# Kernel tuning notes

Hardware: AMD Instinct MI355X
Metric: run time of the kernel (lower is better)

The kernel has to match this reference:

```python
import jax, jax.numpy as jnp
import numpy as np

N = 100000

def _gcn_conv(x, W, b, row, col, norm, n_nodes):
    # x: [N, Fin], W: [Fin, Fout]; message = norm * (x W)[row], aggregated at col
    h = x @ W                                  # small GEMM
    msg = h[row] * norm[:, None]               # [E+N, Fout] gather (memory bound)
    out = jax.ops.segment_sum(msg, col, num_segments=n_nodes)
    return out + b

def _norm_coeffs(edge_index, n_nodes):
    # add self-loops, compute symmetric normalization deg^-1/2[row]*deg^-1/2[col]
    loops = jnp.arange(n_nodes, dtype=edge_index.dtype)
    row = jnp.concatenate([edge_index[0], loops])
    col = jnp.concatenate([edge_index[1], loops])
    deg = jax.ops.segment_sum(jnp.ones_like(col, dtype=jnp.float32), col,
                              num_segments=n_nodes)
    dinv = jnp.where(deg > 0, jax.lax.rsqrt(deg), 0.0)
    norm = dinv[row] * dinv[col]
    return row, col, norm

def setup_inputs() -> dict:
    key = jax.random.key(0)
    ks = jax.random.split(key, 4)
    x = jax.random.normal(ks[0], (N, 64), dtype=jnp.float32)
    edge_index = jax.random.randint(ks[1], (2, 1600000), 0, N, dtype=jnp.int64)
    W1 = jax.random.normal(ks[2], (64, 64), dtype=jnp.float32) / np.sqrt(64)
    b1 = jnp.zeros((64,), dtype=jnp.float32)
    W2 = jax.random.normal(ks[3], (64, 64), dtype=jnp.float32) / np.sqrt(64)
    b2 = jnp.zeros((64,), dtype=jnp.float32)
    return {"x": x, "edge_index": edge_index, "W1": W1, "b1": b1, "W2": W2, "b2": b2}

def reference(x, edge_index, W1, b1, W2, b2):
    row, col, norm = _norm_coeffs(edge_index, N)
    h = jax.nn.relu(_gcn_conv(x, W1, b1, row, col, norm, N))
    return _gcn_conv(h, W2, b2, row, col, norm, N)
```

## Files before the change

### kernel.cpp

```cpp
#include <hip/hip_runtime.h>


#define NPB 32
#define BSH 8
#define BSZ 256
#define PTILE 2048
#define CAP 6144
#define PADALLOW 3856
#define CROW (CAP + PADALLOW)

typedef __attribute__((ext_vector_type(8))) short bf16x8;
typedef __attribute__((ext_vector_type(4))) float f32x4;

__device__ __forceinline__ unsigned bf16_rne(float f) {
    unsigned b = __float_as_uint(f);
    return (b + 0x7fffu + ((b >> 16) & 1u)) >> 16;
}
__device__ __forceinline__ float bf16_lo(unsigned u) { return __uint_as_float(u << 16); }
__device__ __forceinline__ float bf16_hi(unsigned u) { return __uint_as_float(u & 0xffff0000u); }

__global__ void k_binit(int* __restrict__ bcur, int NB) {
    int b = blockIdx.x * blockDim.x + threadIdx.x;
    if (b < NB) bcur[b] = b * CAP;
}

__global__ __launch_bounds__(256) void k_part(const int* __restrict__ rowi,
                                              const int* __restrict__ coli,
                                              int E, int N, int NB, int numTiles,
                                              int* __restrict__ bcur,
                                              unsigned* __restrict__ pairs) {
    __shared__ int hist[512];
    __shared__ int base[512];
    int t = threadIdx.x;
    int T = E + N;
    for (int tile = blockIdx.x; tile < numTiles; tile += gridDim.x) {
        int tstart = tile * PTILE;
        int m = min(PTILE, T - tstart);
        for (int b = t; b < NB; b += 256) hist[b] = 0;
        __syncthreads();
        for (int i = t; i < m; i += 256) {
            int g = tstart + i;
            int c = (g < E) ? coli[g] : (g - E);
            atomicAdd(&hist[c >> BSH], 1);
        }
        __syncthreads();
        for (int b = t; b < NB; b += 256) {
            int h = hist[b];
            base[b] = h ? atomicAdd(&bcur[b], h) : 0;
            hist[b] = 0;
        }
        __syncthreads();
        for (int i = t; i < m; i += 256) {
            int g = tstart + i;
            int r, c;
            if (g < E) { r = rowi[g]; c = coli[g]; }
            else       { r = g - E; c = r; }
            int b = c >> BSH;
            int rank = atomicAdd(&hist[b], 1);
            pairs[base[b] + rank] = (unsigned)r | ((unsigned)(c & (BSZ - 1)) << 24);
        }
        __syncthreads();
    }
}

__global__ __launch_bounds__(1024) void k_bfill(const unsigned* __restrict__ pairs,
                                                const int* __restrict__ bcur,
                                                int N,
                                                int* __restrict__ offsets,
                                                int* __restrict__ cnt,
                                                float* __restrict__ dinv,
                                                int* __restrict__ csrc) {
    __shared__ int scnt[BSZ];
    __shared__ int scur[BSZ];
    __shared__ int wsum[4];
    int b = blockIdx.x;
    int t = threadIdx.x;
    int ebeg = b * CAP;
    int m = bcur[b] - ebeg;
    int pbase = b * CROW;
    if (t < BSZ) scnt[t] = 0;
    __syncthreads();
    for (int i = t; i < m; i += 1024) {
        atomicAdd(&scnt[pairs[ebeg + i] >> 24], 1);
    }
    __syncthreads();
    int cval = 0, pc = 0, inc = 0;
    int lane = t & 63, wid = t >> 6;
    if (t < BSZ) {
        cval = scnt[t];
        pc = (cval + 15) & ~15;
        inc = pc;
        #pragma unroll
        for (int d = 1; d < 64; d <<= 1) {
            int o = __shfl_up(inc, d);
            if (lane >= d) inc += o;
        }
        if (lane == 63) wsum[wid] = inc;
    }
    __syncthreads();
    if (t < BSZ) {
        int woff = 0;
        for (int i = 0; i < wid; i++) woff += wsum[i];
        int off = pbase + woff + inc - pc;
        int v = (b << BSH) + t;
        if (v < N) {
            offsets[v] = off;
            cnt[v] = (cval + 1) & ~1;
            dinv[v] = rsqrtf((float)cval);
        }
        scur[t] = off;
        for (int i = off + cval; i < off + pc; i++) csrc[i] = N;
    }
    __syncthreads();
    for (int i = t; i < m; i += 1024) {
        unsigned pk = pairs[ebeg + i];
        int slot = atomicAdd(&scur[pk >> 24], 1);
        csrc[slot] = (int)(pk & 0xFFFFFFu);
    }
}

template <bool BF16IN>
__global__ __launch_bounds__(256) void k_gemm(const void* __restrict__ Xv,
                                              const float* __restrict__ W,
                                              const float* __restrict__ dinv,
                                              unsigned* __restrict__ Hout,
                                              int N, int nSlabs, int slabStride) {
    __shared__ float SMEM[4224];
    int t = threadIdx.x;
    int lane = t & 63, w = t >> 6;
    int nn = lane & 15, kq = lane >> 4;

    for (int i = t; i < 1024; i += 256) ((float4*)SMEM)[i] = ((const float4*)W)[i];
    __syncthreads();
    bf16x8 Bf[2][4];
    #pragma unroll
    for (int kt = 0; kt < 2; kt++) {
        #pragma unroll
        for (int ct = 0; ct < 4; ct++) {
            union { bf16x8 v; unsigned short s[8]; } u;
            #pragma unroll
            for (int j = 0; j < 8; j++) {
                int k = kt * 32 + kq * 8 + j;
                u.s[j] = (unsigned short)bf16_rne(SMEM[k * 64 + ct * 16 + nn]);
            }
            Bf[kt][ct] = u.v;
        }
    }
    __syncthreads();

    float* outT = SMEM + w * 1056;

    for (int slab = blockIdx.x * 4 + w; slab < nSlabs; slab += slabStride) {
        int row0 = slab * 16;
        int rowA = min(row0 + nn, N - 1);
        bf16x8 A0, A1;
        if (BF16IN) {
            const uint4* X = (const uint4*)Xv;
            union { uint4 u; bf16x8 v; } a0, a1;
            a0.u = X[(size_t)rowA * 8 + kq];
            a1.u = X[(size_t)rowA * 8 + 4 + kq];
            A0 = a0.v; A1 = a1.v;
        } else {
            const float4* X = (const float4*)Xv;
            float4 f0 = X[(size_t)rowA * 16 + kq * 2];
            float4 f1 = X[(size_t)rowA * 16 + kq * 2 + 1];
            float4 f2 = X[(size_t)rowA * 16 + 8 + kq * 2];
            float4 f3 = X[(size_t)rowA * 16 + 8 + kq * 2 + 1];
            union { bf16x8 v; unsigned short s[8]; } a0, a1;
            a0.s[0] = (unsigned short)bf16_rne(f0.x); a0.s[1] = (unsigned short)bf16_rne(f0.y);
            a0.s[2] = (unsigned short)bf16_rne(f0.z); a0.s[3] = (unsigned short)bf16_rne(f0.w);
            a0.s[4] = (unsigned short)bf16_rne(f1.x); a0.s[5] = (unsigned short)bf16_rne(f1.y);
            a0.s[6] = (unsigned short)bf16_rne(f1.z); a0.s[7] = (unsigned short)bf16_rne(f1.w);
            a1.s[0] = (unsigned short)bf16_rne(f2.x); a1.s[1] = (unsigned short)bf16_rne(f2.y);
            a1.s[2] = (unsigned short)bf16_rne(f2.z); a1.s[3] = (unsigned short)bf16_rne(f2.w);
            a1.s[4] = (unsigned short)bf16_rne(f3.x); a1.s[5] = (unsigned short)bf16_rne(f3.y);
            a1.s[6] = (unsigned short)bf16_rne(f3.z); a1.s[7] = (unsigned short)bf16_rne(f3.w);
            A0 = a0.v; A1 = a1.v;
        }
        float dvm = dinv[rowA];

        f32x4 acc[4];
        #pragma unroll
        for (int ct = 0; ct < 4; ct++) acc[ct] = (f32x4){0.f, 0.f, 0.f, 0.f};
        #pragma unroll
        for (int ct = 0; ct < 4; ct++) {
            acc[ct] = __builtin_amdgcn_mfma_f32_16x16x32_bf16(A0, Bf[0][ct], acc[ct], 0, 0, 0);
            acc[ct] = __builtin_amdgcn_mfma_f32_16x16x32_bf16(A1, Bf[1][ct], acc[ct], 0, 0, 0);
        }

        #pragma unroll
        for (int reg = 0; reg < 4; reg++) {
            int r = kq * 4 + reg;
            float dv = __shfl(dvm, r);
            #pragma unroll
            for (int ct = 0; ct < 4; ct++) {
                outT[r * 66 + ct * 16 + nn] = acc[ct][reg] * dv;
            }
        }
        int rr = lane >> 2;
        int c0 = (lane & 3) * 16;
        int orow = row0 + rr;
        if (orow < N) {
            unsigned pk[8];
            #pragma unroll
            for (int i = 0; i < 8; i++) {
                float lo = outT[rr * 66 + c0 + 2 * i];
                float hi = outT[rr * 66 + c0 + 2 * i + 1];
                pk[i] = bf16_rne(lo) | (bf16_rne(hi) << 16);
            }
            uint4* dst = (uint4*)Hout + (size_t)orow * 8 + (lane & 3) * 2;
            dst[0] = make_uint4(pk[0], pk[1], pk[2], pk[3]);
            dst[1] = make_uint4(pk[4], pk[5], pk[6], pk[7]);
        } else if (orow == N) {
            uint4* dst = (uint4*)Hout + (size_t)N * 8 + (lane & 3) * 2;
            dst[0] = make_uint4(0, 0, 0, 0);
            dst[1] = make_uint4(0, 0, 0, 0);
        }
    }
}

template <bool RELU_BF16OUT>
__global__ __launch_bounds__(256) void k_agg(const uint4* __restrict__ H,
                                             const int* __restrict__ offsets,
                                             const int* __restrict__ cnt,
                                             const int* __restrict__ csrc,
                                             const float* __restrict__ dinv,
                                             const float* __restrict__ bias,
                                             void* __restrict__ outv, int N) {
    int t = threadIdx.x;
    int fl = t & 7;
    int v = blockIdx.x * NPB + (t >> 3);
    if (v >= N) return;
    int beg = offsets[v];
    int deg = cnt[v];
    const int2* cs2 = (const int2*)(csrc + beg);
    const char* hb = (const char*)H + ((unsigned)fl << 4);

    float a0 = 0.f, a1 = 0.f, a2 = 0.f, a3 = 0.f;
    float a4 = 0.f, a5 = 0.f, a6 = 0.f, a7 = 0.f;

#define ACC8(R) do {                                                        \
        uint4 dd = *(const uint4*)(hb + ((unsigned)(R) << 7));              \
        a0 += bf16_lo(dd.x); a1 += bf16_hi(dd.x);                           \
        a2 += bf16_lo(dd.y); a3 += bf16_hi(dd.y);                           \
        a4 += bf16_lo(dd.z); a5 += bf16_hi(dd.z);                           \
        a6 += bf16_lo(dd.w); a7 += bf16_hi(dd.w);                           \
    } while (0)

    int2 ss = cs2[0];
    for (int j = 2; j < deg; j += 2) {
        int2 nx = cs2[j >> 1];
        ACC8(ss.x);
        ACC8(ss.y);
        ss = nx;
    }
    ACC8(ss.x);
    ACC8(ss.y);
#undef ACC8

    float dv = dinv[v];
    const float4* b4 = (const float4*)bias;
    float4 bA = b4[fl * 2];
    float4 bB = b4[fl * 2 + 1];
    float r0 = fmaf(dv, a0, bA.x);
    float r1 = fmaf(dv, a1, bA.y);
    float r2 = fmaf(dv, a2, bA.z);
    float r3 = fmaf(dv, a3, bA.w);
    float r4 = fmaf(dv, a4, bB.x);
    float r5 = fmaf(dv, a5, bB.y);
    float r6 = fmaf(dv, a6, bB.z);
    float r7 = fmaf(dv, a7, bB.w);
    if (RELU_BF16OUT) {
        r0 = fmaxf(r0, 0.f); r1 = fmaxf(r1, 0.f);
        r2 = fmaxf(r2, 0.f); r3 = fmaxf(r3, 0.f);
        r4 = fmaxf(r4, 0.f); r5 = fmaxf(r5, 0.f);
        r6 = fmaxf(r6, 0.f); r7 = fmaxf(r7, 0.f);
        uint4 pk;
        pk.x = bf16_rne(r0) | (bf16_rne(r1) << 16);
        pk.y = bf16_rne(r2) | (bf16_rne(r3) << 16);
        pk.z = bf16_rne(r4) | (bf16_rne(r5) << 16);
        pk.w = bf16_rne(r6) | (bf16_rne(r7) << 16);
        ((uint4*)outv)[(size_t)v * 8 + fl] = pk;
    } else {
        float4* o = (float4*)outv + (size_t)v * 16 + fl * 2;
        o[0] = make_float4(r0, r1, r2, r3);
        o[1] = make_float4(r4, r5, r6, r7);
    }
}

extern "C" void kernel_launch(void* const* d_in, const int* in_sizes, int n_in,
                              void* d_out, int out_size, void* d_ws, size_t ws_size,
                              hipStream_t stream) {
    const float* x  = (const float*)d_in[0];
    const int*   ei = (const int*)d_in[1];
    const float* W1 = (const float*)d_in[2];
    const float* b1 = (const float*)d_in[3];
    const float* W2 = (const float*)d_in[4];
    const float* b2 = (const float*)d_in[5];
    float* out      = (float*)d_out;

    const int N = in_sizes[0] / 64;
    const int E = in_sizes[1] / 2;
    const int* row = ei;
    const int* col = ei + E;
    const int T = E + N;
    const int NB = (N + BSZ - 1) >> BSH;

    char* p = (char*)d_ws;
    auto alloc = [&](size_t bytes) { void* r = (void*)p; p += (bytes + 255) & ~(size_t)255; return r; };
    int*      bcur    = (int*)alloc((size_t)(NB + 1) * 4);
    int*      offsets = (int*)alloc((size_t)N * 4);
    int*      cnt     = (int*)alloc((size_t)N * 4);
    float*    dinv    = (float*)alloc((size_t)N * 4);
    unsigned* pairs   = (unsigned*)alloc((size_t)NB * CAP * 4);
    int*      csrc    = (int*)alloc(((size_t)NB * CROW + 64) * 4);
    unsigned* hbuf    = (unsigned*)alloc((size_t)(N + 16) * 32 * 4);
    unsigned* abuf    = (unsigned*)alloc((size_t)(N + 16) * 32 * 4);

    const int numTiles = (T + PTILE - 1) / PTILE;

    k_binit<<<(NB + 255) / 256, 256, 0, stream>>>(bcur, NB);
    k_part<<<numTiles, 256, 0, stream>>>(row, col, E, N, NB, numTiles, bcur, pairs);
    k_bfill<<<NB, 1024, 0, stream>>>(pairs, bcur, N, offsets, cnt, dinv, csrc);

    const int nSlabs = (N + 16) / 16;
    const int GEMM_BLOCKS = 1024;
    const int SLAB_STRIDE = GEMM_BLOCKS * 4;
    const int GB = (N + NPB - 1) / NPB;

    k_gemm<false><<<GEMM_BLOCKS, 256, 0, stream>>>(x, W1, dinv, hbuf, N, nSlabs, SLAB_STRIDE);
    k_agg<true><<<GB, 256, 0, stream>>>((const uint4*)hbuf, offsets, cnt, csrc, dinv, b1, abuf, N);
    k_gemm<true><<<GEMM_BLOCKS, 256, 0, stream>>>(abuf, W2, dinv, hbuf, N, nSlabs, SLAB_STRIDE);
    k_agg<false><<<GB, 256, 0, stream>>>((const uint4*)hbuf, offsets, cnt, csrc, dinv, b2, out, N);
}
```

Measured before the change: 213.8 us.

## Replace atomic bucket partition with count, scan and scatter passes

The single partition kernel, which reserved bucket space with global atomics per tile, becomes three passes: per-tile histograms written to a count matrix, a single-block serial scan over tiles for each bucket, and a scatter using precomputed per-tile bases. The tile size also doubles. This removes global atomic contention on the bucket cursors and the init kernel. In exchange it reads the column indices twice, adds a kernel launch, and uses a serial scan in which each of 391 threads walks about 415 tiles with strided memory accesses, which could be slow.

```diff
diff --git a/kernel.cpp b/kernel.cpp
--- a/kernel.cpp
+++ b/kernel.cpp
@@ -4,7 +4,7 @@
 #define NPB 32
 #define BSH 8
 #define BSZ 256
-#define PTILE 2048
+#define PTILE 4096
 #define CAP 6144
 #define PADALLOW 3856
 #define CROW (CAP + PADALLOW)
@@ -19,52 +19,67 @@
 __device__ __forceinline__ float bf16_lo(unsigned u) { return __uint_as_float(u << 16); }
 __device__ __forceinline__ float bf16_hi(unsigned u) { return __uint_as_float(u & 0xffff0000u); }
 
-__global__ void k_binit(int* __restrict__ bcur, int NB) {
-    int b = blockIdx.x * blockDim.x + threadIdx.x;
-    if (b < NB) bcur[b] = b * CAP;
-}
-
-__global__ __launch_bounds__(256) void k_part(const int* __restrict__ rowi,
-                                              const int* __restrict__ coli,
-                                              int E, int N, int NB, int numTiles,
-                                              int* __restrict__ bcur,
-                                              unsigned* __restrict__ pairs) {
+__global__ __launch_bounds__(256) void k_count(const int* __restrict__ coli,
+                                               int E, int N, int NB, int numTiles,
+                                               int* __restrict__ tcnt) {
     __shared__ int hist[512];
-    __shared__ int base[512];
     int t = threadIdx.x;
     int T = E + N;
-    for (int tile = blockIdx.x; tile < numTiles; tile += gridDim.x) {
-        int tstart = tile * PTILE;
-        int m = min(PTILE, T - tstart);
-        for (int b = t; b < NB; b += 256) hist[b] = 0;
-        __syncthreads();
-        for (int i = t; i < m; i += 256) {
-            int g = tstart + i;
-            int c = (g < E) ? coli[g] : (g - E);
-            atomicAdd(&hist[c >> BSH], 1);
-        }
-        __syncthreads();
-        for (int b = t; b < NB; b += 256) {
-            int h = hist[b];
-            base[b] = h ? atomicAdd(&bcur[b], h) : 0;
-            hist[b] = 0;
-        }
-        __syncthreads();
-        for (int i = t; i < m; i += 256) {
-            int g = tstart + i;
-            int r, c;
-            if (g < E) { r = rowi[g]; c = coli[g]; }
-            else       { r = g - E; c = r; }
-            int b = c >> BSH;
-            int rank = atomicAdd(&hist[b], 1);
-            pairs[base[b] + rank] = (unsigned)r | ((unsigned)(c & (BSZ - 1)) << 24);
-        }
-        __syncthreads();
+    int tile = blockIdx.x;
+    int tstart = tile * PTILE;
+    int m = min(PTILE, T - tstart);
+    for (int b = t; b < NB; b += 256) hist[b] = 0;
+    __syncthreads();
+    for (int i = t; i < m; i += 256) {
+        int g = tstart + i;
+        int c = (g < E) ? coli[g] : (g - E);
+        atomicAdd(&hist[c >> BSH], 1);
+    }
+    __syncthreads();
+    for (int b = t; b < NB; b += 256) tcnt[(size_t)b * numTiles + tile] = hist[b];
+}
+
+__global__ __launch_bounds__(512) void k_scan(int* __restrict__ tcnt,
+                                              int* __restrict__ btot,
+                                              int NB, int numTiles) {
+    int b = threadIdx.x;
+    if (b >= NB) return;
+    int* p = tcnt + (size_t)b * numTiles;
+    int base = b * CAP;
+    for (int t2 = 0; t2 < numTiles; t2++) {
+        int c = p[t2];
+        p[t2] = base;
+        base += c;
+    }
+    btot[b] = base - b * CAP;
+}
+
+__global__ __launch_bounds__(256) void k_scatter(const int* __restrict__ rowi,
+                                                 const int* __restrict__ coli,
+                                                 int E, int N, int NB, int numTiles,
+                                                 const int* __restrict__ tcnt,
+                                                 unsigned* __restrict__ pairs) {
+    __shared__ int scur[512];
+    int t = threadIdx.x;
+    int T = E + N;
+    int tile = blockIdx.x;
+    int tstart = tile * PTILE;
+    int m = min(PTILE, T - tstart);
+    for (int b = t; b < NB; b += 256) scur[b] = tcnt[(size_t)b * numTiles + tile];
+    __syncthreads();
+    for (int i = t; i < m; i += 256) {
+        int g = tstart + i;
+        int r, c;
+        if (g < E) { r = rowi[g]; c = coli[g]; }
+        else       { r = g - E; c = r; }
+        int b = c >> BSH;
+        int slot = atomicAdd(&scur[b], 1);
+        pairs[slot] = (unsigned)r | ((unsigned)(c & (BSZ - 1)) << 24);
     }
 }
 
 __global__ __launch_bounds__(1024) void k_bfill(const unsigned* __restrict__ pairs,
-                                                const int* __restrict__ bcur,
+                                                const int* __restrict__ btot,
                                                 int N,
                                                 int* __restrict__ offsets,
                                                 int* __restrict__ cnt,
@@ -76,7 +91,7 @@
     int b = blockIdx.x;
     int t = threadIdx.x;
     int ebeg = b * CAP;
-    int m = bcur[b] - ebeg;
+    int m = btot[b];
     int pbase = b * CROW;
     if (t < BSZ) scnt[t] = 0;
     __syncthreads();
@@ -305,10 +320,12 @@
     const int* col = ei + E;
     const int T = E + N;
     const int NB = (N + BSZ - 1) >> BSH;
+    const int numTiles = (T + PTILE - 1) / PTILE;
 
     char* p = (char*)d_ws;
     auto alloc = [&](size_t bytes) { void* r = (void*)p; p += (bytes + 255) & ~(size_t)255; return r; };
-    int*      bcur    = (int*)alloc((size_t)(NB + 1) * 4);
+    int*      tcnt    = (int*)alloc((size_t)NB * numTiles * 4);
+    int*      btot    = (int*)alloc((size_t)(NB + 1) * 4);
     int*      offsets = (int*)alloc((size_t)N * 4);
     int*      cnt     = (int*)alloc((size_t)N * 4);
     float*    dinv    = (float*)alloc((size_t)N * 4);
@@ -317,11 +334,10 @@
     unsigned* hbuf    = (unsigned*)alloc((size_t)(N + 16) * 32 * 4);
     unsigned* abuf    = (unsigned*)alloc((size_t)(N + 16) * 32 * 4);
 
-    const int numTiles = (T + PTILE - 1) / PTILE;
-
-    k_binit<<<(NB + 255) / 256, 256, 0, stream>>>(bcur, NB);
-    k_part<<<numTiles, 256, 0, stream>>>(row, col, E, N, NB, numTiles, bcur, pairs);
-    k_bfill<<<NB, 1024, 0, stream>>>(pairs, bcur, N, offsets, cnt, dinv, csrc);
+    k_count<<<numTiles, 256, 0, stream>>>(col, E, N, NB, numTiles, tcnt);
+    k_scan<<<1, 512, 0, stream>>>(tcnt, btot, NB, numTiles);
+    k_scatter<<<numTiles, 256, 0, stream>>>(row, col, E, N, NB, numTiles, tcnt, pairs);
+    k_bfill<<<NB, 1024, 0, stream>>>(pairs, btot, N, offsets, cnt, dinv, csrc);
 
     const int nSlabs = (N + 16) / 16;
     const int GEMM_BLOCKS = 1024;
```

After: 421.6 us. 1.97x slower.
